# Optimization experiments

Measured on AMD Instinct MI355X. Metric: run time of the kernel, lower is better.

The kernel has to match this reference:

```python
import math
import jax, jax.numpy as jnp
import numpy as np

B, N, D_MODEL, H = 2, 4096, 2048, 16
HEAD_DIM = D_MODEL // H
CHUNK = 128  # chunk length for the lightning-attention recurrence


def _slopes(n_heads):
    # ALiBi-style slopes used by lightning attention (n_heads is a power of 2)
    start = 2.0 ** (-(2.0 ** -(math.log2(n_heads) - 3)))
    return np.array([start ** (i + 1) for i in range(n_heads)], dtype=np.float32)


def setup_inputs() -> dict:
    key = jax.random.key(0)
    kx, k1, k2, k3, k4 = jax.random.split(key, 5)
    scale = 1.0 / math.sqrt(D_MODEL)
    x = jax.random.normal(kx, (B, N, D_MODEL), dtype=jnp.float32)
    w_qkv = jax.random.normal(k1, (3 * D_MODEL, D_MODEL), dtype=jnp.float32) * scale
    b_qkv = jax.random.normal(k2, (3 * D_MODEL,), dtype=jnp.float32) * 0.01
    w_out = jax.random.normal(k3, (D_MODEL, D_MODEL), dtype=jnp.float32) * scale
    b_out = jax.random.normal(k4, (D_MODEL,), dtype=jnp.float32) * 0.01
    return {"x": x, "w_qkv": w_qkv, "b_qkv": b_qkv, "w_out": w_out, "b_out": b_out}


def _lightning_attn(q, k, v):
    # q,k,v: (B, H, N, d). Causal linear attention with per-head decay lam:
    #   S_t = lam * S_{t-1} + k_t v_t^T ;  o_t = q_t S_t
    b, h, n, d = q.shape
    nc = n // CHUNK
    lam = jnp.exp(-jnp.asarray(_slopes(h)))  # (H,)

    pos = jnp.arange(CHUNK, dtype=jnp.float32)
    decay_q = lam[:, None] ** (pos + 1.0)            # (H, C) inter-chunk q scaling
    decay_k = lam[:, None] ** (CHUNK - 1.0 - pos)    # (H, C) state-update k scaling
    diff = pos[:, None] - pos[None, :]
    causal = diff >= 0
    dmask = jnp.where(causal, lam[:, None, None] ** jnp.maximum(diff, 0.0), 0.0)  # (H,C,C)
    lam_c = lam ** CHUNK                              # (H,)

    def to_chunks(t):
        return t.reshape(b, h, nc, CHUNK, d).transpose(2, 0, 1, 3, 4)  # (nc,B,H,C,d)

    qc, kc, vc = to_chunks(q), to_chunks(k), to_chunks(v)

    def step(S, inp):
        qb, kb, vb = inp  # each (B,H,C,d); S: (B,H,d,d)
        inter = jnp.einsum('bhcd,bhde->bhce', qb * decay_q[None, :, :, None], S)
        scores = jnp.einsum('bhcd,bhed->bhce', qb, kb) * dmask[None]
        intra = jnp.einsum('bhce,bhed->bhcd', scores, vb)
        S_new = lam_c[None, :, None, None] * S + jnp.einsum(
            'bhcd,bhce->bhde', kb * decay_k[None, :, :, None], vb)
        return S_new, inter + intra

    S0 = jnp.zeros((b, h, d, d), dtype=q.dtype)
    _, out = jax.lax.scan(step, S0, (qc, kc, vc))  # out: (nc,B,H,C,d)
    return out.transpose(1, 2, 0, 3, 4).reshape(b, h, n, d)


def reference(x, w_qkv, b_qkv, w_out, b_out):
    b, n, dm = x.shape
    qkv = x @ w_qkv.T + b_qkv                         # (B,N,3D)
    q, k, v = jnp.split(qkv, 3, axis=-1)
    def heads(t):
        return t.reshape(b, n, H, HEAD_DIM).transpose(0, 2, 1, 3)  # (B,H,N,d)
    attn = _lightning_attn(heads(q), heads(k), heads(v))
    attn = attn.transpose(0, 2, 1, 3).reshape(b, n, dm)
    return attn @ w_out.T + b_out
```

## Files before the change

kernel.cpp:

```cpp
#include <hip/hip_runtime.h>
#include <stdint.h>

#define DM    2048
#define NSEQ  4096
#define BB    2
#define NH    16
#define HD    128
#define CHK   128
#define NCHK  32
#define NBH   (BB*NH)
#define MTOT  (BB*NSEQ)
#define N3    (3*DM)

typedef unsigned short u16;
typedef unsigned int   u32;
typedef __attribute__((ext_vector_type(8))) short s16x8;
typedef __attribute__((ext_vector_type(4))) short s16x4;
typedef __attribute__((ext_vector_type(4))) float f32x4;
typedef __attribute__((ext_vector_type(2))) unsigned short u16x2;

__device__ __forceinline__ float b2f(u16 b){ u32 u = ((u32)b) << 16; float f; __builtin_memcpy(&f,&u,4); return f; }
__device__ __forceinline__ u16 f2b(float f){ u32 u; __builtin_memcpy(&u,&f,4); u += 0x7fffu + ((u>>16)&1u); return (u16)(u>>16); }

__device__ __forceinline__ void gload16(const u16* g, u16* l){
  __builtin_amdgcn_global_load_lds((const __attribute__((address_space(1))) void*)g,
                                   (__attribute__((address_space(3))) void*)l, 16, 0, 0);
}

__global__ __launch_bounds__(256) void conv_bf16(const float* __restrict__ src,
                                                 u16* __restrict__ dst, int n4)
{
  for (int i = blockIdx.x*blockDim.x + threadIdx.x; i < n4; i += gridDim.x*blockDim.x){
    f32x4 v = *(const f32x4*)(src + (size_t)i*4);
    s16x4 o;
    #pragma unroll
    for (int j=0;j<4;j++) o[j] = (short)f2b(v[j]);
    *(s16x4*)(dst + (size_t)i*4) = o;
  }
}


#define GEMM256_CORE(GA_, GB_)                                                  \
  const int tid  = threadIdx.x;                                                 \
  const int lane = tid & 63;                                                    \
  const int w    = tid >> 6;                                                    \
  const int wm_i = w >> 2, wn_i = w & 3;                                        \
  const int m0 = blockIdx.y << 8;                                               \
  const int n0 = blockIdx.x << 8;                                               \
         \
  const int q_  = (lane*16) ^ (((lane>>5)&1) << 5);                             \
  const int sgr = q_ >> 6;                                                      \
  const int sgc = (q_ & 63) >> 1;                                               \
  const u16* gA = GA_ + (size_t)(m0 + w*32 + sgr)*DM + sgc;                     \
  const u16* gB = GB_ + (size_t)(n0 + w*32 + sgr)*DM + sgc;                     \
  const int l15 = lane & 15, lg = lane >> 4;                                    \
  const int swz = ((lg*16) ^ (((l15>>3)&1) << 5)) >> 1;          \
  const int arow = (wm_i*128 + l15)*32 + swz;                                   \
  const int brow = (wn_i*64  + l15)*32 + swz;                                   \
  f32x4 acc[8][4];                                                              \
  _Pragma("unroll")                                                             \
  for (int m=0;m<8;m++)                                                         \
    _Pragma("unroll")                                                           \
    for (int n=0;n<4;n++) acc[m][n] = f32x4{0.f,0.f,0.f,0.f};                   \
  auto STAGE = [&](int set, int kt){                                            \
    const u16* a = gA + kt*32;                                                  \
    const u16* b = gB + kt*32;                                                  \
    u16* la = lds + set + w*1024;                                               \
    gload16(a,         la);                                                     \
    gload16(a + 16*DM, la + 512);                                               \
    gload16(b,         la + 8192);                                              \
    gload16(b + 16*DM, la + 8704);                                              \
  };                                                                            \
  auto COMPUTE = [&](int set){                                                  \
    const u16* base = lds + set;                                                \
    s16x8 af[8], bf[4];                                                         \
    _Pragma("unroll")                                                           \
    for (int m=0;m<8;m++) af[m] = *(const s16x8*)(base + arow + m*512);         \
    _Pragma("unroll")                                                           \
    for (int n=0;n<4;n++) bf[n] = *(const s16x8*)(base + 8192 + brow + n*512);  \
    __builtin_amdgcn_s_setprio(1);                                              \
    _Pragma("unroll")                                                           \
    for (int m=0;m<8;m++)                                                       \
      _Pragma("unroll")                                                         \
      for (int n=0;n<4;n++)                                                     \
        acc[m][n] = __builtin_amdgcn_mfma_f32_16x16x32_bf16(af[m], bf[n], acc[m][n], 0,0,0); \
    __builtin_amdgcn_s_setprio(0);                                              \
  };                                                                            \
  STAGE(0, 0); STAGE(16384, 1); STAGE(32768, 2);                                \
  asm volatile("s_waitcnt vmcnt(8)" ::: "memory");                              \
  __builtin_amdgcn_s_barrier();                                                 \
  int s0=0, s1=16384, s2=32768, s3=49152;                                       \
  for (int t=0; t<64; ++t){                                                     \
    if (t < 61) STAGE(s3, t+3);                                                 \
    COMPUTE(s0);                                                                \
    if      (t < 61)  { asm volatile("s_waitcnt vmcnt(8)" ::: "memory"); }      \
    else if (t == 61) { asm volatile("s_waitcnt vmcnt(4)" ::: "memory"); }      \
    else if (t == 62) { asm volatile("s_waitcnt vmcnt(0)" ::: "memory"); }      \
    __builtin_amdgcn_s_barrier();                                               \
    const int tmp=s0; s0=s1; s1=s2; s2=s3; s3=tmp;                              \
  }

__global__ __launch_bounds__(512, 2) void gemm_qkv(const u16* __restrict__ Xb,
    const u16* __restrict__ Wb, const float* __restrict__ bias,
    u16* __restrict__ Qb, u16* __restrict__ Kb, u16* __restrict__ Vb)
{
  __shared__ u16 lds[4*16384];
  GEMM256_CORE(Xb, Wb)

  #pragma unroll
  for (int n=0;n<4;n++){
    const int gn = n0 + wn_i*64 + n*16 + l15;
    const float bv = bias[gn];
    const int which = gn >> 11;
    const int h = (gn >> 7) & 15;
    const int e = gn & 127;
    u16* base_ = (which==0) ? Qb : ((which==1) ? Kb : Vb);
    #pragma unroll
    for (int m=0;m<8;m++){
      #pragma unroll
      for (int r=0;r<4;r++){
        const int gm = m0 + wm_i*128 + m*16 + lg*4 + r;
        const int b  = gm >> 12;
        const int tt = gm & (NSEQ-1);
        base_[(((size_t)(b*NH + h))*NSEQ + tt)*HD + e] = f2b(acc[m][n][r] + bv);
      }
    }
  }
}

__global__ __launch_bounds__(512, 2) void gemm_out(const u16* __restrict__ Ab,
    const u16* __restrict__ Wb, const float* __restrict__ bias,
    float* __restrict__ Out)
{
  __shared__ u16 lds[4*16384];
  GEMM256_CORE(Ab, Wb)

  #pragma unroll
  for (int n=0;n<4;n++){
    const int gn = n0 + wn_i*64 + n*16 + l15;
    const float bv = bias[gn];
    #pragma unroll
    for (int m=0;m<8;m++){
      #pragma unroll
      for (int r=0;r<4;r++){
        const int gm = m0 + wm_i*128 + m*16 + lg*4 + r;
        Out[(size_t)gm*DM + gn] = acc[m][n][r] + bv;
      }
    }
  }
}

__global__ __launch_bounds__(256) void chunk_kv(const u16* __restrict__ Kb,
    const u16* __restrict__ Vb, u16* __restrict__ USb)
{
  __shared__ short Kt[128][152];
  __shared__ short Vt[128][152];
  const int tid = threadIdx.x;
  const int blk = blockIdx.x;
  const int c  = blk & (NCHK-1);
  const int bh = blk >> 5;
  const int h  = bh & (NH-1);
  const float slope = exp2f(-0.5f*(float)(h+1));

  const u16* kg = Kb + ((size_t)bh*NSEQ + (size_t)c*CHK)*HD;
  const u16* vg = Vb + ((size_t)bh*NSEQ + (size_t)c*CHK)*HD;

  const int e0 = (tid & 63) * 2;
  const int tq = tid >> 6;
  #pragma unroll
  for (int it=0; it<4; it++){
    const int tb = it*32 + tq*8;
    s16x8 k0v, k1v, v0v, v1v;
    #pragma unroll
    for (int j=0;j<8;j++){
      const int t = tb + j;
      u16x2 kv = *(const u16x2*)(kg + (size_t)t*HD + e0);
      u16x2 vv = *(const u16x2*)(vg + (size_t)t*HD + e0);
      const float dk = expf(-slope*(float)(CHK-1-t));
      k0v[j] = (short)f2b(b2f(kv[0])*dk);
      k1v[j] = (short)f2b(b2f(kv[1])*dk);
      v0v[j] = (short)vv[0];
      v1v[j] = (short)vv[1];
    }
    *(s16x8*)&Kt[e0  ][tb] = k0v;
    *(s16x8*)&Kt[e0+1][tb] = k1v;
    *(s16x8*)&Vt[e0  ][tb] = v0v;
    *(s16x8*)&Vt[e0+1][tb] = v1v;
  }
  __syncthreads();

  const int lane = tid & 63;
  const int l15 = lane & 15, lg = lane >> 4;
  const int w = tid >> 6;
  const int wm = (w >> 1) << 6, wn = (w & 1) << 6;
  f32x4 acc[4][4];
  #pragma unroll
  for (int i=0;i<4;i++)
    #pragma unroll
    for (int j=0;j<4;j++) acc[i][j] = f32x4{0.f,0.f,0.f,0.f};

  #pragma unroll
  for (int ks=0; ks<4; ks++){
    const int kk = ks*32 + lg*8;
    s16x8 af[4], bf[4];
    #pragma unroll
    for (int m=0;m<4;m++) af[m] = *(const s16x8*)&Kt[wm + m*16 + l15][kk];
    #pragma unroll
    for (int n=0;n<4;n++) bf[n] = *(const s16x8*)&Vt[wn + n*16 + l15][kk];
    #pragma unroll
    for (int m=0;m<4;m++)
      #pragma unroll
      for (int n=0;n<4;n++)
        acc[m][n] = __builtin_amdgcn_mfma_f32_16x16x32_bf16(af[m], bf[n], acc[m][n], 0,0,0);
  }

  u16* up = USb + (size_t)blk*(HD*HD);
  #pragma unroll
  for (int m=0;m<4;m++)
    #pragma unroll
    for (int n=0;n<4;n++)
      #pragma unroll
      for (int r=0;r<4;r++){
        const int d = wm + m*16 + lg*4 + r;
        const int f = wn + n*16 + l15;
        up[d*HD + f] = f2b(acc[m][n][r]);
      }
}

__global__ __launch_bounds__(256) void scan_state(u16* __restrict__ USb)
{
  const int bh = blockIdx.x >> 3;
  const int rs = blockIdx.x & 7;
  const int tid = threadIdx.x;
  const int h = bh & (NH-1);
  const float slope = exp2f(-0.5f*(float)(h+1));
  const float lamC = expf(-slope*(float)CHK);
  float s[8];
  #pragma unroll
  for (int i=0;i<8;i++) s[i]=0.f;
  u16* base = USb + (size_t)bh*NCHK*HD*HD + rs*2048;
  const int off = tid*8;
  for (int c=0;c<NCHK;c++){
    u16* p = base + (size_t)c*HD*HD + off;
    s16x8 u = *(const s16x8*)p;
    s16x8 wv;
    #pragma unroll
    for (int j=0;j<8;j++) wv[j] = (short)f2b(s[j]);
    *(s16x8*)p = wv;
    #pragma unroll
    for (int j=0;j<8;j++) s[j] = lamC*s[j] + b2f((u16)u[j]);
  }
}

__global__ __launch_bounds__(512) void attn_chunk(
    const u16* __restrict__ Qb, const u16* __restrict__ Kb, const u16* __restrict__ Vb,
    const u16* __restrict__ Sb, u16* __restrict__ ATT)
{
  __shared__ short lds[73728];
  short* Qs = lds;
  short* Ks = lds + 17408;
  short* Vt = lds + 34816;
  short* St = lds + 54272;

  const int tid = threadIdx.x;
  const int blk = blockIdx.x;
  const int c  = blk & (NCHK-1);
  const int bh = blk >> 5;
  const int b  = bh >> 4, h = bh & 15;
  const float slope = exp2f(-0.5f*(float)(h+1));

  const size_t qoff = ((size_t)bh*NSEQ + (size_t)c*CHK)*HD;

  #pragma unroll
  for (int i=0;i<4;i++){
    const int lin = i*4096 + tid*8;
    const int r = lin >> 7, e = lin & 127;
    *(s16x8*)&Qs[r*136 + e] = *(const s16x8*)(Qb + qoff + lin);
    *(s16x8*)&Ks[r*136 + e] = *(const s16x8*)(Kb + qoff + lin);
  }
  {
    const int f0 = (tid & 63)*2;
    const int tq = tid >> 6;
    const u16* vg = Vb + qoff;
    const u16* sg = Sb + ((size_t)bh*NCHK + c)*HD*HD;
    #pragma unroll
    for (int it=0; it<2; it++){
      const int t0 = it*64 + tq*8;
      s16x8 v0v, v1v, s0v, s1v;
      #pragma unroll
      for (int j=0;j<8;j++){
        u16x2 v2 = *(const u16x2*)(vg + (size_t)(t0+j)*HD + f0);
        u16x2 s2 = *(const u16x2*)(sg + (size_t)(t0+j)*HD + f0);
        v0v[j]=(short)v2[0]; v1v[j]=(short)v2[1];
        s0v[j]=(short)s2[0]; s1v[j]=(short)s2[1];
      }
      *(s16x8*)&Vt[(f0  )*152 + t0] = v0v;
      *(s16x8*)&Vt[(f0+1)*152 + t0] = v1v;
      *(s16x8*)&St[(f0  )*152 + t0] = s0v;
      *(s16x8*)&St[(f0+1)*152 + t0] = s1v;
    }
  }
  __syncthreads();

  const int lane = tid & 63;
  const int l15 = lane & 15, lg = lane >> 4;
  const int w = tid >> 6;
  const int wrow = (w >> 1) << 5;
  const int wcol = (w & 1) << 6;

  f32x4 accs[2][4], acco[2][4];
  #pragma unroll
  for (int m=0;m<2;m++)
    #pragma unroll
    for (int n=0;n<4;n++){ accs[m][n]=f32x4{0.f,0.f,0.f,0.f}; acco[m][n]=f32x4{0.f,0.f,0.f,0.f}; }

  #pragma unroll
  for (int ks=0; ks<4; ks++){
    const int kk = ks*32 + lg*8;
    s16x8 qa[2], kb_[4], sb_[4];
    #pragma unroll
    for (int m=0;m<2;m++) qa[m] = *(const s16x8*)&Qs[(wrow + m*16 + l15)*136 + kk];
    #pragma unroll
    for (int n=0;n<4;n++){
      kb_[n] = *(const s16x8*)&Ks[(wcol + n*16 + l15)*136 + kk];
      sb_[n] = *(const s16x8*)&St[(wcol + n*16 + l15)*152 + kk];
    }
    #pragma unroll
    for (int m=0;m<2;m++)
      #pragma unroll
      for (int n=0;n<4;n++){
        accs[m][n] = __builtin_amdgcn_mfma_f32_16x16x32_bf16(qa[m], kb_[n], accs[m][n], 0,0,0);
        acco[m][n] = __builtin_amdgcn_mfma_f32_16x16x32_bf16(qa[m], sb_[n], acco[m][n], 0,0,0);
      }
  }
  __syncthreads();

  #pragma unroll
  for (int m=0;m<2;m++){
    #pragma unroll
    for (int r=0;r<4;r++){
      const int t = wrow + m*16 + lg*4 + r;
      const float dq = expf(-slope*(float)(t+1));
      #pragma unroll
      for (int n=0;n<4;n++){
        const int s = wcol + n*16 + l15;
        float v = accs[m][n][r];
        v = (t >= s) ? v*expf(-slope*(float)(t-s)) : 0.f;
        Ks[t*136 + s] = (short)f2b(v);
        acco[m][n][r] *= dq;
      }
    }
  }
  __syncthreads();

  #pragma unroll
  for (int ks=0; ks<4; ks++){
    const int kk = ks*32 + lg*8;
    s16x8 sa[2], vb_[4];
    #pragma unroll
    for (int m=0;m<2;m++) sa[m] = *(const s16x8*)&Ks[(wrow + m*16 + l15)*136 + kk];
    #pragma unroll
    for (int n=0;n<4;n++) vb_[n] = *(const s16x8*)&Vt[(wcol + n*16 + l15)*152 + kk];
    #pragma unroll
    for (int m=0;m<2;m++)
      #pragma unroll
      for (int n=0;n<4;n++)
        acco[m][n] = __builtin_amdgcn_mfma_f32_16x16x32_bf16(sa[m], vb_[n], acco[m][n], 0,0,0);
  }

  u16* op = ATT + ((size_t)(b*NSEQ + c*CHK))*DM + h*HD;
  #pragma unroll
  for (int m=0;m<2;m++)
    #pragma unroll
    for (int n=0;n<4;n++)
      #pragma unroll
      for (int r=0;r<4;r++){
        const int t = wrow + m*16 + lg*4 + r;
        const int f = wcol + n*16 + l15;
        op[(size_t)t*DM + f] = f2b(acco[m][n][r]);
      }
}

extern "C" void kernel_launch(void* const* d_in, const int* in_sizes, int n_in,
                              void* d_out, int out_size, void* d_ws, size_t ws_size,
                              hipStream_t stream)
{
  const float* x     = (const float*)d_in[0];
  const float* w_qkv = (const float*)d_in[1];
  const float* b_qkv = (const float*)d_in[2];
  const float* w_out = (const float*)d_in[3];
  const float* b_out = (const float*)d_in[4];
  float* out = (float*)d_out;

  char* ws = (char*)d_ws;
  const size_t SZ = (size_t)MTOT * DM * sizeof(u16);
  u16* Qb    = (u16*)(ws);
  u16* Kb    = (u16*)(ws + SZ);
  u16* Vb    = (u16*)(ws + 2*SZ);
  u16* USb   = (u16*)(ws + 3*SZ);
  u16* ATT   = (u16*)(ws + 4*SZ);
  u16* Xb    = ATT;
  u16* Wqkvb = USb;
  u16* Woutb = Kb;

  conv_bf16 <<<dim3(2048), 256, 0, stream>>>(x,     Xb,    MTOT*DM/4);
  conv_bf16 <<<dim3(2048), 256, 0, stream>>>(w_qkv, Wqkvb, N3*DM/4);
  gemm_qkv  <<<dim3(N3/256,  MTOT/256), 512, 0, stream>>>(Xb, Wqkvb, b_qkv, Qb, Kb, Vb);
  chunk_kv  <<<dim3(NBH*NCHK),          256, 0, stream>>>(Kb, Vb, USb);
  scan_state<<<dim3(NBH*8),             256, 0, stream>>>(USb);
  attn_chunk<<<dim3(NBH*NCHK),          512, 0, stream>>>(Qb, Kb, Vb, USb, ATT);
  conv_bf16 <<<dim3(1024), 256, 0, stream>>>(w_out, Woutb, DM*DM/4);
  gemm_out  <<<dim3(DM/256,  MTOT/256), 512, 0, stream>>>(ATT, Woutb, b_out, out);
}
```

Baseline: 403.0 us.

## Restructure GEMM mainloop to K=64 tiles with phased staging and XOR swizzle

```diff
diff --git a/kernel.cpp b/kernel.cpp
--- a/kernel.cpp
+++ b/kernel.cpp
@@ -41,70 +41,97 @@
 
 
 #define GEMM256_CORE(GA_, GB_)                                                  \
+  __shared__ u16 lds[65536];                                       \
   const int tid  = threadIdx.x;                                                 \
   const int lane = tid & 63;                                                    \
   const int w    = tid >> 6;                                                    \
   const int wm_i = w >> 2, wn_i = w & 3;                                        \
   const int m0 = blockIdx.y << 8;                                               \
   const int n0 = blockIdx.x << 8;                                               \
-         \
-  const int q_  = (lane*16) ^ (((lane>>5)&1) << 5);                             \
-  const int sgr = q_ >> 6;                                                      \
-  const int sgc = (q_ & 63) >> 1;                                               \
-  const u16* gA = GA_ + (size_t)(m0 + w*32 + sgr)*DM + sgc;                     \
-  const u16* gB = GB_ + (size_t)(n0 + w*32 + sgr)*DM + sgc;                     \
-  const int l15 = lane & 15, lg = lane >> 4;                                    \
-  const int swz = ((lg*16) ^ (((l15>>3)&1) << 5)) >> 1;          \
-  const int arow = (wm_i*128 + l15)*32 + swz;                                   \
-  const int brow = (wn_i*64  + l15)*32 + swz;                                   \
+  const int l15 = lane & 15, lg = lane >> 4, l7 = lane & 7;                     \
+  const int c0 = ((lg)     ^ l7) << 3;                      \
+  const int c1 = ((4 + lg) ^ l7) << 3;                      \
+  const int abase = wm_i*8192 + l15*64;                                         \
+  const int bbase = 32768 + (wn_i>>1)*8192 + (wn_i&1)*4096 + l15*64;            \
+  const int grow = lane >> 3;                                                   \
+  const int gcol = ((lane & 7) ^ grow) * 8;                                     \
+  const u16* gAl = GA_ + (size_t)(m0 + grow)*DM + gcol;                         \
+  const u16* gBl = GB_ + (size_t)(n0 + grow)*DM + gcol;                         \
+  auto STG = [&](const u16* gl, int ldsbase, int h, int kt){                    \
+    _Pragma("unroll")                                                           \
+    for (int j=0;j<2;j++)                                                       \
+      gload16(gl + ((size_t)(h*128 + j*64 + w*8))*DM + (size_t)kt*64,           \
+              lds + ldsbase + (j*64 + w*8)*64);                                 \
+  };                                                                            \
   f32x4 acc[8][4];                                                              \
   _Pragma("unroll")                                                             \
   for (int m=0;m<8;m++)                                                         \
     _Pragma("unroll")                                                           \
     for (int n=0;n<4;n++) acc[m][n] = f32x4{0.f,0.f,0.f,0.f};                   \
-  auto STAGE = [&](int set, int kt){                                            \
-    const u16* a = gA + kt*32;                                                  \
-    const u16* b = gB + kt*32;                                                  \
-    u16* la = lds + set + w*1024;                                               \
-    gload16(a,         la);                                                     \
-    gload16(a + 16*DM, la + 512);                                               \
-    gload16(b,         la + 8192);                                              \
-    gload16(b + 16*DM, la + 8704);                                              \
-  };                                                                            \
-  auto COMPUTE = [&](int set){                                                  \
-    const u16* base = lds + set;                                                \
-    s16x8 af[8], bf[4];                                                         \
+  s16x8 bfr[4][2];                                                              \
+         \
+  STG(gBl, 32768,             0, 0); STG(gBl, 32768+8192,       1, 0);          \
+  STG(gAl, 0,                 0, 0); STG(gAl, 8192,             1, 0);          \
+  STG(gBl, 32768+16384,       0, 1); STG(gBl, 32768+16384+8192, 1, 1);          \
+  asm volatile("s_waitcnt vmcnt(4)" ::: "memory");                              \
+  __builtin_amdgcn_s_barrier();                                                 \
+  for (int it=0; it<15; ++it){                                                  \
+    const int k1 = 2*it+1, k2 = 2*it+2, k3 = 2*it+3;                            \
+    PH(0,0, STG(gAl, 16384,             0, k1), );                              \
+    PH(0,1, STG(gAl, 16384+8192,        1, k1), );                              \
+    PH(0,2, STG(gBl, 32768,             0, k2), );                              \
+    PH(0,3, STG(gBl, 32768+8192,        1, k2),                                 \
+            asm volatile("s_waitcnt vmcnt(4)" ::: "memory"));                   \
+    PH(1,0, STG(gAl, 0,                 0, k2), );                              \
+    PH(1,1, STG(gAl, 8192,              1, k2), );                              \
+    PH(1,2, STG(gBl, 32768+16384,       0, k3), );                              \
+    PH(1,3, STG(gBl, 32768+16384+8192,  1, k3),                                 \
+            asm volatile("s_waitcnt vmcnt(4)" ::: "memory"));                   \
+  }                                                                             \
+                      \
+  PH(0,0, STG(gAl, 16384,      0, 31), );                                       \
+  PH(0,1, STG(gAl, 16384+8192, 1, 31), );                                       \
+  PH(0,2, (void)0, );                                                           \
+  PH(0,3, (void)0, asm volatile("s_waitcnt vmcnt(0)" ::: "memory"));            \
+  PH(1,0, (void)0, ); PH(1,1, (void)0, );                                       \
+  PH(1,2, (void)0, ); PH(1,3, (void)0, );
+
+#define PH(D, Q, STAGE, VM) do{                                                 \
+  s16x8 af[2][2];                                                               \
+  if ((Q)==0){                                                                  \
     _Pragma("unroll")                                                           \
-    for (int m=0;m<8;m++) af[m] = *(const s16x8*)(base + arow + m*512);         \
+    for (int n=0;n<4;n++){                                                      \
+      bfr[n][0] = *(const s16x8*)(lds + bbase + (D)*16384 + n*1024 + c0);       \
+      bfr[n][1] = *(const s16x8*)(lds + bbase + (D)*16384 + n*1024 + c1);       \
+    }                                                                           \
+  }                                                                             \
+  af[0][0] = *(const s16x8*)(lds + abase + (D)*16384 + (2*(Q)  )*1024 + c0);    \
+  af[0][1] = *(const s16x8*)(lds + abase + (D)*16384 + (2*(Q)  )*1024 + c1);    \
+  af[1][0] = *(const s16x8*)(lds + abase + (D)*16384 + (2*(Q)+1)*1024 + c0);    \
+  af[1][1] = *(const s16x8*)(lds + abase + (D)*16384 + (2*(Q)+1)*1024 + c1);    \
+  STAGE;                                                                        \
+  if ((Q)==0) asm volatile("s_waitcnt lgkmcnt(8)" ::: "memory");                \
+  __builtin_amdgcn_s_barrier();                                                 \
+  asm volatile("s_waitcnt lgkmcnt(0)" ::: "memory");                            \
+  __builtin_amdgcn_sched_barrier(0);                                            \
+  __builtin_amdgcn_s_setprio(1);                                                \
+  _Pragma("unroll")                                                             \
+  for (int kk=0;kk<2;kk++)                                                      \
     _Pragma("unroll")                                                           \
-    for (int n=0;n<4;n++) bf[n] = *(const s16x8*)(base + 8192 + brow + n*512);  \
-    __builtin_amdgcn_s_setprio(1);                                              \
-    _Pragma("unroll")                                                           \
-    for (int m=0;m<8;m++)                                                       \
+    for (int mm=0;mm<2;mm++)                                                    \
       _Pragma("unroll")                                                         \
       for (int n=0;n<4;n++)                                                     \
-        acc[m][n] = __builtin_amdgcn_mfma_f32_16x16x32_bf16(af[m], bf[n], acc[m][n], 0,0,0); \
-    __builtin_amdgcn_s_setprio(0);                                              \
-  };                                                                            \
-  STAGE(0, 0); STAGE(16384, 1); STAGE(32768, 2);                                \
-  asm volatile("s_waitcnt vmcnt(8)" ::: "memory");                              \
+        acc[2*(Q)+mm][n] = __builtin_amdgcn_mfma_f32_16x16x32_bf16(             \
+            af[mm][kk], bfr[n][kk], acc[2*(Q)+mm][n], 0,0,0);                   \
+  __builtin_amdgcn_s_setprio(0);                                                \
+  VM;                                                                           \
   __builtin_amdgcn_s_barrier();                                                 \
-  int s0=0, s1=16384, s2=32768, s3=49152;                                       \
-  for (int t=0; t<64; ++t){                                                     \
-    if (t < 61) STAGE(s3, t+3);                                                 \
-    COMPUTE(s0);                                                                \
-    if      (t < 61)  { asm volatile("s_waitcnt vmcnt(8)" ::: "memory"); }      \
-    else if (t == 61) { asm volatile("s_waitcnt vmcnt(4)" ::: "memory"); }      \
-    else if (t == 62) { asm volatile("s_waitcnt vmcnt(0)" ::: "memory"); }      \
-    __builtin_amdgcn_s_barrier();                                               \
-    const int tmp=s0; s0=s1; s1=s2; s2=s3; s3=tmp;                              \
-  }
+}while(0)
 
 __global__ __launch_bounds__(512, 2) void gemm_qkv(const u16* __restrict__ Xb,
     const u16* __restrict__ Wb, const float* __restrict__ bias,
     u16* __restrict__ Qb, u16* __restrict__ Kb, u16* __restrict__ Vb)
 {
-  __shared__ u16 lds[4*16384];
   GEMM256_CORE(Xb, Wb)
 
   #pragma unroll
@@ -132,7 +159,6 @@
     const u16* __restrict__ Wb, const float* __restrict__ bias,
     float* __restrict__ Out)
 {
-  __shared__ u16 lds[4*16384];
   GEMM256_CORE(Ab, Wb)
 
   #pragma unroll
@@ -256,11 +282,11 @@
     const u16* __restrict__ Qb, const u16* __restrict__ Kb, const u16* __restrict__ Vb,
     const u16* __restrict__ Sb, u16* __restrict__ ATT)
 {
-  __shared__ short lds[73728];
-  short* Qs = lds;
-  short* Ks = lds + 17408;
-  short* Vt = lds + 34816;
-  short* St = lds + 54272;
+  __shared__ short alds[73728];
+  short* Qs = alds;
+  short* Ks = alds + 17408;
+  short* Vt = alds + 34816;
+  short* St = alds + 54272;
 
   const int tid = threadIdx.x;
   const int blk = blockIdx.x;
```

Result: faster. 377.2 us (-6.4%).
